# Kernel tuning notes

Measured on AMD Instinct MI355X. Metric: run time of the kernel, lower is better.

Reference implementation:

```python
import jax, jax.numpy as jnp
import numpy as np

UB = 35.0      # per-coordinate upper bound
SUM = 150.0    # equality constraint sum(z) = 150
NEG_SLOPE = 0.2


def _qp_project_one(v):
    """Solve min_z 0.5||z||^2 - v^T z  s.t. 0<=z<=UB, sum(z)=SUM  (n=5).
    Solution: z_i = clip(v_i - nu, 0, UB) with nu s.t. sum(z)=SUM.
    Exact closed form via the piecewise-linear breakpoints of g(nu)=sum(clip(v-nu,0,UB)).
    This matches QPFunction(Q=I, p=x, G,h box, A,b simplex) with v = -x."""
    bp = jnp.concatenate([v, v - UB])              # [10] breakpoints of g(nu)
    bs = jnp.sort(bp)[::-1]                        # descending in nu; g nondecreasing
    mid = 0.5 * (bs[:-1] + bs[1:])                 # [9] segment midpoints
    free = (v[None, :] > mid[:, None]) & (v[None, :] < mid[:, None] + UB)
    upper = v[None, :] >= mid[:, None] + UB
    nfree = jnp.sum(free, axis=1)
    num = jnp.sum(jnp.where(free, v[None, :], 0.0), axis=1) + UB * jnp.sum(upper, axis=1) - SUM
    nu_cand = num / jnp.maximum(nfree, 1)
    valid = (nfree > 0) & (nu_cand <= bs[:-1] + 1e-6) & (nu_cand >= bs[1:] - 1e-6)
    nu = nu_cand[jnp.argmax(valid)]
    return jnp.clip(v - nu, 0.0, UB)


def setup_inputs() -> dict:
    key = jax.random.key(0)
    ks = jax.random.split(key, 7)
    B, S, A = 65536, 17, 5
    state = jax.random.normal(ks[0], (B, S), dtype=jnp.float32)
    W1 = jax.random.normal(ks[1], (400, S), dtype=jnp.float32) * 0.05
    b1 = jax.random.normal(ks[2], (400,), dtype=jnp.float32) * 0.05
    W2 = jax.random.normal(ks[3], (300, 400), dtype=jnp.float32) * 0.05
    b2 = jax.random.normal(ks[4], (300,), dtype=jnp.float32) * 0.05
    W3 = jax.random.normal(ks[5], (A, 300), dtype=jnp.float32) * 0.05
    b3 = jax.random.normal(ks[6], (A,), dtype=jnp.float32) * 0.05
    return {"state": state, "W1": W1, "b1": b1, "W2": W2, "b2": b2,
            "W3": W3, "b3": b3, "training": 0}


def reference(state, W1, b1, W2, b2, W3, b3, training):
    lrelu = lambda x: jax.nn.leaky_relu(x, NEG_SLOPE)
    a = lrelu(state @ W1.T + b1)
    a = lrelu(a @ W2.T + b2)
    scaled_a = lrelu(a @ W3.T + b3)            # [B, 5]
    # QPFunction is called with linear term p = scaled_a, so v = -scaled_a
    opt_a = jax.vmap(_qp_project_one)(-scaled_a)
    return opt_a
```

## Files before the change

kernel.cpp:

```cpp
#include <hip/hip_runtime.h>
#include <hip/hip_bf16.h>

typedef __bf16 bf16x8 __attribute__((ext_vector_type(8)));
typedef float  f32x4  __attribute__((ext_vector_type(4)));
typedef long   long2v __attribute__((ext_vector_type(2)));

#define UBV   35.0f
#define SUMC  150.0f

__device__ __forceinline__ float lrelu(float x) { return fmaxf(x, 0.2f * x); }

__device__ __forceinline__ unsigned pkword(float a, float b, float c, float d) {
    unsigned w = (unsigned)__builtin_amdgcn_cvt_pk_fp8_f32(a, b, 0, false);
    w = (unsigned)__builtin_amdgcn_cvt_pk_fp8_f32(c, d, (int)w, true);
    return w;
}
__device__ __forceinline__ long mk64(unsigned lo, unsigned hi) {
    return (long)(((unsigned long long)hi << 32) | (unsigned long long)lo);
}
__device__ __forceinline__ void async16(void* lds_uniform, const void* gsrc) {
    __builtin_amdgcn_global_load_lds(
        (__attribute__((address_space(1))) void*)(gsrc),
        (__attribute__((address_space(3))) void*)(lds_uniform),
        16, 0, 0);
}


__global__ void prep_kernel(const float* __restrict__ W1, const float* __restrict__ b1,
                            const float* __restrict__ W2, const float* __restrict__ b2,
                            const float* __restrict__ W3, const float* __restrict__ b3,
                            __bf16* __restrict__ w1p, uint2* __restrict__ w2p,
                            uint2* __restrict__ w3c)
{
    int idx = blockIdx.x * blockDim.x + threadIdx.x;
    if (idx < 1664) {
        int lane = idx & 63;
        int nt = idx >> 6;
        int c16 = lane & 15, g = lane >> 4;
        int kk = nt >> 1, hh = nt & 1;
        int kap = kk * 32 + (c16 >> 2) * 8 + hh * 4 + (c16 & 3);
        bf16x8 v;
        #pragma unroll
        for (int j = 0; j < 8; ++j) {
            int k = g * 8 + j;
            float x = 0.f;
            if (kap < 400) {
                if (k < 17) x = W1[kap * 17 + k];
                else if (k == 17) x = b1[kap];
            } else if (kap == 400) {
                if (k == 17) x = 1.0f;
            }
            v[j] = (__bf16)x;
        }
        *(bf16x8*)(w1p + idx * 8) = v;
    } else if (idx < 1664 + 16640) {
        int i2 = idx - 1664;
        int fg = i2 >> 6, lane = i2 & 63;
        int q = fg / 65, rem = fg % 65;
        int t = rem / 13, kt = rem % 13;
        int c16 = lane & 15, g = lane >> 4;
        int local = t * 16 + c16;
        int ff = q * 79 + local;
        float v[8];
        #pragma unroll
        for (int j = 0; j < 8; ++j) {
            int kap = kt * 32 + g * 8 + j;
            float x = 0.f;
            if (local == 79) {
                x = (kap == 400) ? 1.0f : 0.f;
            } else if (local < 79 && ff < 300) {
                if (kap < 400) x = W2[ff * 400 + kap];
                else if (kap == 400) x = b2[ff];
            }
            v[j] = x;
        }
        uint2 d;
        d.x = pkword(v[0], v[1], v[2], v[3]);
        d.y = pkword(v[4], v[5], v[6], v[7]);
        int within = (kt < 12) ? ((kt >> 1) * 128 + lane * 2 + (kt & 1))
                               : (768 + lane);
        w2p[(q * 5 + t) * 832 + within] = d;
    } else if (idx < 1664 + 16640 + 768) {
        int i3 = idx - 1664 - 16640;
        int fg = i3 >> 6, lane = i3 & 63;
        int q = fg / 3, k2 = fg % 3;
        int o = lane & 15, g = lane >> 4;
        float v[8];
        #pragma unroll
        for (int j = 0; j < 8; ++j) {
            int t2  = 2 * k2 + (j >> 2);
            int rho = g * 4 + (j & 3);
            int local = t2 * 16 + rho;
            float x = 0.f;
            if (o < 5 && t2 < 5) {
                if (local == 79) x = b3[o] * 0.25f;
                else if (local < 79 && q * 79 + local < 300)
                    x = W3[o * 300 + q * 79 + local];
            }
            v[j] = x;
        }
        uint2 d;
        d.x = pkword(v[0], v[1], v[2], v[3]);
        d.y = pkword(v[4], v[5], v[6], v[7]);
        w3c[i3] = d;
    }
}

__global__ __launch_bounds__(256, 1)
void actor_kernel(const float* __restrict__ state,
                  const __bf16* __restrict__ w1p,
                  const uint2* __restrict__ w2p,
                  const uint2* __restrict__ w3c,
                  float* __restrict__ out)
{
    __shared__ __align__(16) char s_mem[2][33792];

    const int tid = threadIdx.x;
    const int wid = tid >> 6;
    const int ln  = tid & 63;
    const int g   = ln >> 4, c16 = ln & 15;
    const int brow = blockIdx.x << 7;

    {
        const char* gb1 = (const char*)w1p;
        #pragma unroll
        for (int i = wid; i < 26; i += 4)
            async16(&s_mem[0][0] + i * 1024, gb1 + i * 1024 + ln * 16);
        const char* gb2 = (const char*)w2p;
        #pragma unroll
        for (int i = wid; i < 33; i += 4)
            async16(&s_mem[1][0] + i * 1024, gb2 + i * 1024 + ln * 16);
    }

    bf16x8 sbA, sbB;
    {
        const float* spA = state + (brow + wid * 32 + c16) * 17;
        const float* spB = spA + 16 * 17;
        if (g == 0) {
            #pragma unroll
            for (int j = 0; j < 8; ++j) { sbA[j] = (__bf16)spA[j]; sbB[j] = (__bf16)spB[j]; }
        } else if (g == 1) {
            #pragma unroll
            for (int j = 0; j < 8; ++j) { sbA[j] = (__bf16)spA[8 + j]; sbB[j] = (__bf16)spB[8 + j]; }
        } else if (g == 2) {
            sbA[0] = (__bf16)spA[16]; sbB[0] = (__bf16)spB[16];
            sbA[1] = (__bf16)1.0f;    sbB[1] = (__bf16)1.0f;
            #pragma unroll
            for (int j = 2; j < 8; ++j) { sbA[j] = (__bf16)0.f; sbB[j] = (__bf16)0.f; }
        } else {
            #pragma unroll
            for (int j = 0; j < 8; ++j) { sbA[j] = (__bf16)0.f; sbB[j] = (__bf16)0.f; }
        }
    }

    long w3r[4][3];
    {
        const long* gw3 = (const long*)w3c;
        #pragma unroll
        for (int q = 0; q < 4; ++q)
            #pragma unroll
            for (int k2 = 0; k2 < 3; ++k2)
                w3r[q][k2] = gw3[(q * 3 + k2) * 64 + ln];
    }

    __syncthreads();

    long frvA[13], frvB[13];
    #pragma unroll
    for (int kt = 0; kt < 13; ++kt) {
        bf16x8 we = *(const bf16x8*)(&s_mem[0][0] + ((2 * kt) * 64 + ln) * 16);
        bf16x8 wo = *(const bf16x8*)(&s_mem[0][0] + ((2 * kt + 1) * 64 + ln) * 16);
        f32x4 aeA = {0.f,0.f,0.f,0.f}, aoA = {0.f,0.f,0.f,0.f};
        f32x4 aeB = {0.f,0.f,0.f,0.f}, aoB = {0.f,0.f,0.f,0.f};
        aeA = __builtin_amdgcn_mfma_f32_16x16x32_bf16(we, sbA, aeA, 0, 0, 0);
        aoA = __builtin_amdgcn_mfma_f32_16x16x32_bf16(wo, sbA, aoA, 0, 0, 0);
        aeB = __builtin_amdgcn_mfma_f32_16x16x32_bf16(we, sbB, aeB, 0, 0, 0);
        aoB = __builtin_amdgcn_mfma_f32_16x16x32_bf16(wo, sbB, aoB, 0, 0, 0);
        frvA[kt] = mk64(
            pkword(lrelu(aeA[0]), lrelu(aeA[1]), lrelu(aeA[2]), lrelu(aeA[3])),
            pkword(lrelu(aoA[0]), lrelu(aoA[1]), lrelu(aoA[2]), lrelu(aoA[3])));
        frvB[kt] = mk64(
            pkword(lrelu(aeB[0]), lrelu(aeB[1]), lrelu(aeB[2]), lrelu(aeB[3])),
            pkword(lrelu(aoB[0]), lrelu(aoB[1]), lrelu(aoB[2]), lrelu(aoB[3])));
    }

    __syncthreads();

    f32x4 ccsA = {0.f, 0.f, 0.f, 0.f};
    f32x4 ccsB = {0.f, 0.f, 0.f, 0.f};

    #pragma unroll 1
    for (int q = 0; q < 4; ++q) {
        if (q < 3) {
            char* lb = &s_mem[q & 1][0];
            const char* gb = (const char*)w2p + (q + 1) * 33280;
            #pragma unroll
            for (int i = wid; i < 33; i += 4)
                async16(lb + i * 1024, gb + i * 1024 + ln * 16);
        }

        const char* bufp = &s_mem[(q & 1) ^ 1][0];
        unsigned wdA[5], wdB[5];
        #pragma unroll
        for (int t = 0; t < 5; ++t) {
            const char* bt = bufp + t * 6656;
            f32x4 aA = {0.f,0.f,0.f,0.f}, aB = {0.f,0.f,0.f,0.f};
            #pragma unroll
            for (int kt2 = 0; kt2 < 6; ++kt2) {
                long2v p = *(const long2v*)(bt + kt2 * 1024 + ln * 16);
                aA = __builtin_amdgcn_mfma_f32_16x16x32_fp8_fp8(p[0], frvA[2 * kt2],     aA, 0, 0, 0);
                aB = __builtin_amdgcn_mfma_f32_16x16x32_fp8_fp8(p[0], frvB[2 * kt2],     aB, 0, 0, 0);
                aA = __builtin_amdgcn_mfma_f32_16x16x32_fp8_fp8(p[1], frvA[2 * kt2 + 1], aA, 0, 0, 0);
                aB = __builtin_amdgcn_mfma_f32_16x16x32_fp8_fp8(p[1], frvB[2 * kt2 + 1], aB, 0, 0, 0);
            }
            long p12 = *(const long*)(bt + 6144 + ln * 8);
            aA = __builtin_amdgcn_mfma_f32_16x16x32_fp8_fp8(p12, frvA[12], aA, 0, 0, 0);
            aB = __builtin_amdgcn_mfma_f32_16x16x32_fp8_fp8(p12, frvB[12], aB, 0, 0, 0);
            wdA[t] = pkword(lrelu(aA[0]), lrelu(aA[1]), lrelu(aA[2]), lrelu(aA[3]));
            wdB[t] = pkword(lrelu(aB[0]), lrelu(aB[1]), lrelu(aB[2]), lrelu(aB[3]));
        }
        {
            f32x4 cc = {0.f, 0.f, 0.f, 0.f};
            cc = __builtin_amdgcn_mfma_f32_16x16x32_fp8_fp8(w3r[q][0], mk64(wdA[0], wdA[1]), cc, 0, 0, 0);
            cc = __builtin_amdgcn_mfma_f32_16x16x32_fp8_fp8(w3r[q][1], mk64(wdA[2], wdA[3]), cc, 0, 0, 0);
            cc = __builtin_amdgcn_mfma_f32_16x16x32_fp8_fp8(w3r[q][2], mk64(wdA[4], 0u),     cc, 0, 0, 0);
            ccsA += cc;
        }
        {
            f32x4 cc = {0.f, 0.f, 0.f, 0.f};
            cc = __builtin_amdgcn_mfma_f32_16x16x32_fp8_fp8(w3r[q][0], mk64(wdB[0], wdB[1]), cc, 0, 0, 0);
            cc = __builtin_amdgcn_mfma_f32_16x16x32_fp8_fp8(w3r[q][1], mk64(wdB[2], wdB[3]), cc, 0, 0, 0);
            cc = __builtin_amdgcn_mfma_f32_16x16x32_fp8_fp8(w3r[q][2], mk64(wdB[4], 0u),     cc, 0, 0, 0);
            ccsB += cc;
        }
        if (q < 3) __syncthreads();
    }

    float tA4 = __shfl_xor(ccsA[0], 16);
    float sB0 = __shfl_xor(ccsB[0], 16);
    float sB1 = __shfl_xor(ccsB[1], 16);
    float sB2 = __shfl_xor(ccsB[2], 16);
    float sB3 = __shfl_xor(ccsB[3], 16);

    if (ln < 32) {
        float v[5];
        if (ln < 16) {
            v[0] = -lrelu(ccsA[0]); v[1] = -lrelu(ccsA[1]);
            v[2] = -lrelu(ccsA[2]); v[3] = -lrelu(ccsA[3]);
            v[4] = -lrelu(tA4);
        } else {
            v[0] = -lrelu(sB0); v[1] = -lrelu(sB1);
            v[2] = -lrelu(sB2); v[3] = -lrelu(sB3);
            v[4] = -lrelu(ccsB[0]);
        }

        float bp[10];
        #pragma unroll
        for (int i = 0; i < 5; ++i) { bp[i] = v[i]; bp[i + 5] = v[i] - UBV; }
        float blo = -1e30f, glo = 0.f;
        #pragma unroll
        for (int j = 0; j < 10; ++j) {
            float b = bp[j];
            float gsum = 0.f;
            #pragma unroll
            for (int i = 0; i < 5; ++i) {
                float zc = v[i] - b;
                zc = fminf(fmaxf(zc, 0.f), UBV);
                gsum += zc;
            }
            if (gsum >= SUMC && b > blo) { blo = b; glo = gsum; }
        }
        float bhi = 1e30f;
        #pragma unroll
        for (int j = 0; j < 10; ++j) {
            float b = bp[j];
            if (b > blo && b < bhi) bhi = b;
        }
        float mid = 0.5f * (blo + bhi);
        int nfree = 0;
        #pragma unroll
        for (int i = 0; i < 5; ++i)
            nfree += (v[i] > mid && v[i] < mid + UBV) ? 1 : 0;
        float nu = (nfree > 0) ? blo + (glo - SUMC) / (float)nfree : blo;

        int row = brow + wid * 32 + ln;
        #pragma unroll
        for (int o = 0; o < 5; ++o) {
            float zf = v[o] - nu;
            zf = fminf(fmaxf(zf, 0.f), UBV);
            out[row * 5 + o] = zf;
        }
    }
}

extern "C" void kernel_launch(void* const* d_in, const int* in_sizes, int n_in,
                              void* d_out, int out_size, void* d_ws, size_t ws_size,
                              hipStream_t stream) {
    const float* state = (const float*)d_in[0];
    const float* W1    = (const float*)d_in[1];
    const float* b1    = (const float*)d_in[2];
    const float* W2    = (const float*)d_in[3];
    const float* b2    = (const float*)d_in[4];
    const float* W3    = (const float*)d_in[5];
    const float* b3    = (const float*)d_in[6];
    float* out = (float*)d_out;

    char* base = (char*)d_ws;
    __bf16* w1p = (__bf16*)base;
    uint2*  w2p = (uint2*)(base + 26624);
    uint2*  w3c = (uint2*)(base + 26624 + 133120);

    const int total = 1664 + 16640 + 768;
    prep_kernel<<<(total + 255) / 256, 256, 0, stream>>>(W1, b1, W2, b2, W3, b3,
                                                         w1p, w2p, w3c);

    int B = in_sizes[0] / 17;
    actor_kernel<<<B / 128, 256, 0, stream>>>(state, w1p, w2p, w3c, out);
}
```

Baseline: 28.59 us.

## Split layer-2 output quarters across two wave groups with LDS reduction

After: 30.41 us. 1.06x slower.

```diff
diff --git a/kernel.cpp b/kernel.cpp
--- a/kernel.cpp
+++ b/kernel.cpp
@@ -106,35 +106,33 @@
     }
 }
 
-__global__ __launch_bounds__(256, 1)
+__global__ __launch_bounds__(512, 4)
 void actor_kernel(const float* __restrict__ state,
                   const __bf16* __restrict__ w1p,
                   const uint2* __restrict__ w2p,
                   const uint2* __restrict__ w3c,
                   float* __restrict__ out)
 {
-    __shared__ __align__(16) char s_mem[2][33792];
+    __shared__ __align__(16) char s_buf[2][33792];
+    __shared__ float s_red[2][4][32][8];
 
     const int tid = threadIdx.x;
     const int wid = tid >> 6;
     const int ln  = tid & 63;
     const int g   = ln >> 4, c16 = ln & 15;
-    const int brow = blockIdx.x << 7;
-
-    {
-        const char* gb1 = (const char*)w1p;
-        #pragma unroll
-        for (int i = wid; i < 26; i += 4)
-            async16(&s_mem[0][0] + i * 1024, gb1 + i * 1024 + ln * 16);
-        const char* gb2 = (const char*)w2p;
-        #pragma unroll
-        for (int i = wid; i < 33; i += 4)
-            async16(&s_mem[1][0] + i * 1024, gb2 + i * 1024 + ln * 16);
+    const int rg  = wid & 3;
+    const int qh  = wid >> 2;
+    const int brow = (blockIdx.x << 7) + rg * 32;
+
+    for (int b = 0; b < 2; ++b) {
+        const char* gb = (const char*)w2p + (b * 2) * 33280;
+        for (int i = wid; i < 33; i += 8)
+            async16(&s_buf[b][0] + i * 1024, gb + i * 1024 + ln * 16);
     }
 
     bf16x8 sbA, sbB;
     {
-        const float* spA = state + (brow + wid * 32 + c16) * 17;
+        const float* spA = state + (brow + c16) * 17;
         const float* spB = spA + 16 * 17;
         if (g == 0) {
             #pragma unroll
@@ -153,23 +151,21 @@
         }
     }
 
-    long w3r[4][3];
+    long w3r[2][3];
     {
         const long* gw3 = (const long*)w3c;
         #pragma unroll
-        for (int q = 0; q < 4; ++q)
+        for (int qi = 0; qi < 2; ++qi)
             #pragma unroll
             for (int k2 = 0; k2 < 3; ++k2)
-                w3r[q][k2] = gw3[(q * 3 + k2) * 64 + ln];
-    }
-
-    __syncthreads();
+                w3r[qi][k2] = gw3[((qh * 2 + qi) * 3 + k2) * 64 + ln];
+    }
 
     long frvA[13], frvB[13];
     #pragma unroll
     for (int kt = 0; kt < 13; ++kt) {
-        bf16x8 we = *(const bf16x8*)(&s_mem[0][0] + ((2 * kt) * 64 + ln) * 16);
-        bf16x8 wo = *(const bf16x8*)(&s_mem[0][0] + ((2 * kt + 1) * 64 + ln) * 16);
+        bf16x8 we = *(const bf16x8*)(w1p + ((2 * kt) * 64 + ln) * 8);
+        bf16x8 wo = *(const bf16x8*)(w1p + ((2 * kt + 1) * 64 + ln) * 8);
         f32x4 aeA = {0.f,0.f,0.f,0.f}, aoA = {0.f,0.f,0.f,0.f};
         f32x4 aeB = {0.f,0.f,0.f,0.f}, aoB = {0.f,0.f,0.f,0.f};
         aeA = __builtin_amdgcn_mfma_f32_16x16x32_bf16(we, sbA, aeA, 0, 0, 0);
@@ -186,21 +182,9 @@
 
     __syncthreads();
 
-    f32x4 ccsA = {0.f, 0.f, 0.f, 0.f};
-    f32x4 ccsB = {0.f, 0.f, 0.f, 0.f};
-
-    #pragma unroll 1
-    for (int q = 0; q < 4; ++q) {
-        if (q < 3) {
-            char* lb = &s_mem[q & 1][0];
-            const char* gb = (const char*)w2p + (q + 1) * 33280;
-            #pragma unroll
-            for (int i = wid; i < 33; i += 4)
-                async16(lb + i * 1024, gb + i * 1024 + ln * 16);
-        }
-
-        const char* bufp = &s_mem[(q & 1) ^ 1][0];
-        unsigned wdA[5], wdB[5];
+    unsigned wdA[5], wdB[5];
+    auto consume_q = [&]() {
+        const char* bufp = &s_buf[qh][0];
         #pragma unroll
         for (int t = 0; t < 5; ++t) {
             const char* bt = bufp + t * 6656;
@@ -219,39 +203,56 @@
             wdA[t] = pkword(lrelu(aA[0]), lrelu(aA[1]), lrelu(aA[2]), lrelu(aA[3]));
             wdB[t] = pkword(lrelu(aB[0]), lrelu(aB[1]), lrelu(aB[2]), lrelu(aB[3]));
         }
-        {
-            f32x4 cc = {0.f, 0.f, 0.f, 0.f};
-            cc = __builtin_amdgcn_mfma_f32_16x16x32_fp8_fp8(w3r[q][0], mk64(wdA[0], wdA[1]), cc, 0, 0, 0);
-            cc = __builtin_amdgcn_mfma_f32_16x16x32_fp8_fp8(w3r[q][1], mk64(wdA[2], wdA[3]), cc, 0, 0, 0);
-            cc = __builtin_amdgcn_mfma_f32_16x16x32_fp8_fp8(w3r[q][2], mk64(wdA[4], 0u),     cc, 0, 0, 0);
-            ccsA += cc;
-        }
-        {
-            f32x4 cc = {0.f, 0.f, 0.f, 0.f};
-            cc = __builtin_amdgcn_mfma_f32_16x16x32_fp8_fp8(w3r[q][0], mk64(wdB[0], wdB[1]), cc, 0, 0, 0);
-            cc = __builtin_amdgcn_mfma_f32_16x16x32_fp8_fp8(w3r[q][1], mk64(wdB[2], wdB[3]), cc, 0, 0, 0);
-            cc = __builtin_amdgcn_mfma_f32_16x16x32_fp8_fp8(w3r[q][2], mk64(wdB[4], 0u),     cc, 0, 0, 0);
-            ccsB += cc;
-        }
-        if (q < 3) __syncthreads();
-    }
-
-    float tA4 = __shfl_xor(ccsA[0], 16);
-    float sB0 = __shfl_xor(ccsB[0], 16);
-    float sB1 = __shfl_xor(ccsB[1], 16);
-    float sB2 = __shfl_xor(ccsB[2], 16);
-    float sB3 = __shfl_xor(ccsB[3], 16);
-
-    if (ln < 32) {
+    };
+    auto fold_q = [&](int qi, f32x4& cA, f32x4& cB) {
+        f32x4 cc = {0.f, 0.f, 0.f, 0.f};
+        cc = __builtin_amdgcn_mfma_f32_16x16x32_fp8_fp8(w3r[qi][0], mk64(wdA[0], wdA[1]), cc, 0, 0, 0);
+        cc = __builtin_amdgcn_mfma_f32_16x16x32_fp8_fp8(w3r[qi][1], mk64(wdA[2], wdA[3]), cc, 0, 0, 0);
+        cc = __builtin_amdgcn_mfma_f32_16x16x32_fp8_fp8(w3r[qi][2], mk64(wdA[4], 0u),     cc, 0, 0, 0);
+        cA += cc;
+        f32x4 cd = {0.f, 0.f, 0.f, 0.f};
+        cd = __builtin_amdgcn_mfma_f32_16x16x32_fp8_fp8(w3r[qi][0], mk64(wdB[0], wdB[1]), cd, 0, 0, 0);
+        cd = __builtin_amdgcn_mfma_f32_16x16x32_fp8_fp8(w3r[qi][1], mk64(wdB[2], wdB[3]), cd, 0, 0, 0);
+        cd = __builtin_amdgcn_mfma_f32_16x16x32_fp8_fp8(w3r[qi][2], mk64(wdB[4], 0u),     cd, 0, 0, 0);
+        cB += cd;
+    };
+
+    f32x4 ccsA = {0.f, 0.f, 0.f, 0.f};
+    f32x4 ccsB = {0.f, 0.f, 0.f, 0.f};
+
+    consume_q();
+    __syncthreads();
+
+    for (int b = 0; b < 2; ++b) {
+        const char* gb = (const char*)w2p + (b * 2 + 1) * 33280;
+        for (int i = wid; i < 33; i += 8)
+            async16(&s_buf[b][0] + i * 1024, gb + i * 1024 + ln * 16);
+    }
+    fold_q(0, ccsA, ccsB);
+
+    __syncthreads();
+
+    consume_q();
+    fold_q(1, ccsA, ccsB);
+
+    if (g == 0) {
+        #pragma unroll
+        for (int o = 0; o < 4; ++o) {
+            s_red[qh][rg][c16][o]      = ccsA[o];
+            s_red[qh][rg][16 + c16][o] = ccsB[o];
+        }
+    } else if (g == 1) {
+        s_red[qh][rg][c16][4]      = ccsA[0];
+        s_red[qh][rg][16 + c16][4] = ccsB[0];
+    }
+    __syncthreads();
+
+    if (qh == 0 && ln < 32) {
         float v[5];
-        if (ln < 16) {
-            v[0] = -lrelu(ccsA[0]); v[1] = -lrelu(ccsA[1]);
-            v[2] = -lrelu(ccsA[2]); v[3] = -lrelu(ccsA[3]);
-            v[4] = -lrelu(tA4);
-        } else {
-            v[0] = -lrelu(sB0); v[1] = -lrelu(sB1);
-            v[2] = -lrelu(sB2); v[3] = -lrelu(sB3);
-            v[4] = -lrelu(ccsB[0]);
+        #pragma unroll
+        for (int o = 0; o < 5; ++o) {
+            float s = s_red[0][rg][ln][o] + s_red[1][rg][ln][o];
+            v[o] = -lrelu(s);
         }
 
         float bp[10];
@@ -283,7 +284,7 @@
             nfree += (v[i] > mid && v[i] < mid + UBV) ? 1 : 0;
         float nu = (nfree > 0) ? blo + (glo - SUMC) / (float)nfree : blo;
 
-        int row = brow + wid * 32 + ln;
+        int row = brow + ln;
         #pragma unroll
         for (int o = 0; o < 5; ++o) {
             float zf = v[o] - nu;
@@ -315,5 +316,5 @@
                                                          w1p, w2p, w3c);
 
     int B = in_sizes[0] / 17;
-    actor_kernel<<<B / 128, 256, 0, stream>>>(state, w1p, w2p, w3c, out);
-}
+    actor_kernel<<<B / 128, 512, 0, stream>>>(state, w1p, w2p, w3c, out);
+}
```

## Use 16x16x128 scaled FP8 MFMA for layer-2 with re-laid-out weights

Applied to the files above, without the earlier changes.

Measured after the change: 26.67 us. -6.7%, faster.

```diff
diff --git a/kernel.cpp b/kernel.cpp
--- a/kernel.cpp
+++ b/kernel.cpp
@@ -4,9 +4,11 @@
 typedef __bf16 bf16x8 __attribute__((ext_vector_type(8)));
 typedef float  f32x4  __attribute__((ext_vector_type(4)));
 typedef long   long2v __attribute__((ext_vector_type(2)));
+typedef int    int8v  __attribute__((ext_vector_type(8)));
 
 #define UBV   35.0f
 #define SUMC  150.0f
+#define SCL1  0x7f7f7f7f
 
 __device__ __forceinline__ float lrelu(float x) { return fmaxf(x, 0.2f * x); }
 
@@ -36,9 +38,10 @@
     if (idx < 1664) {
         int lane = idx & 63;
         int nt = idx >> 6;
-        int c16 = lane & 15, g = lane >> 4;
-        int kk = nt >> 1, hh = nt & 1;
-        int kap = kk * 32 + (c16 >> 2) * 8 + hh * 4 + (c16 & 3);
+        int rho = lane & 15, g = lane >> 4;
+        int kap = (nt < 24)
+            ? 128 * (nt >> 3) + 32 * (rho >> 2) + 4 * (nt & 7) + (rho & 3)
+            : 384 + 8 * (rho >> 2) + 4 * (nt & 1) + (rho & 3);
         bf16x8 v;
         #pragma unroll
         for (int j = 0; j < 8; ++j) {
@@ -61,10 +64,19 @@
         int c16 = lane & 15, g = lane >> 4;
         int local = t * 16 + c16;
         int ff = q * 79 + local;
+        int within, kbase;
+        if (kt < 12) {
+            int m = kt >> 2, u = kt & 3;
+            kbase = 128 * m + 32 * g + 8 * u;
+            within = m * 256 + lane * 4 + u;
+        } else {
+            kbase = 384 + g * 8;
+            within = 768 + lane;
+        }
         float v[8];
         #pragma unroll
         for (int j = 0; j < 8; ++j) {
-            int kap = kt * 32 + g * 8 + j;
+            int kap = kbase + j;
             float x = 0.f;
             if (local == 79) {
                 x = (kap == 400) ? 1.0f : 0.f;
@@ -77,8 +89,6 @@
         uint2 d;
         d.x = pkword(v[0], v[1], v[2], v[3]);
         d.y = pkword(v[4], v[5], v[6], v[7]);
-        int within = (kt < 12) ? ((kt >> 1) * 128 + lane * 2 + (kt & 1))
-                               : (768 + lane);
         w2p[(q * 5 + t) * 832 + within] = d;
     } else if (idx < 1664 + 16640 + 768) {
         int i3 = idx - 1664 - 16640;
@@ -113,7 +123,7 @@
                   const uint2* __restrict__ w3c,
                   float* __restrict__ out)
 {
-    __shared__ __align__(16) char s_mem[2][33792];
+    __shared__ __align__(32) char s_mem[2][33792];
 
     const int tid = threadIdx.x;
     const int wid = tid >> 6;
@@ -165,23 +175,35 @@
 
     __syncthreads();
 
-    long frvA[13], frvB[13];
-    #pragma unroll
-    for (int kt = 0; kt < 13; ++kt) {
-        bf16x8 we = *(const bf16x8*)(&s_mem[0][0] + ((2 * kt) * 64 + ln) * 16);
-        bf16x8 wo = *(const bf16x8*)(&s_mem[0][0] + ((2 * kt + 1) * 64 + ln) * 16);
-        f32x4 aeA = {0.f,0.f,0.f,0.f}, aoA = {0.f,0.f,0.f,0.f};
-        f32x4 aeB = {0.f,0.f,0.f,0.f}, aoB = {0.f,0.f,0.f,0.f};
-        aeA = __builtin_amdgcn_mfma_f32_16x16x32_bf16(we, sbA, aeA, 0, 0, 0);
-        aoA = __builtin_amdgcn_mfma_f32_16x16x32_bf16(wo, sbA, aoA, 0, 0, 0);
-        aeB = __builtin_amdgcn_mfma_f32_16x16x32_bf16(we, sbB, aeB, 0, 0, 0);
-        aoB = __builtin_amdgcn_mfma_f32_16x16x32_bf16(wo, sbB, aoB, 0, 0, 0);
-        frvA[kt] = mk64(
-            pkword(lrelu(aeA[0]), lrelu(aeA[1]), lrelu(aeA[2]), lrelu(aeA[3])),
-            pkword(lrelu(aoA[0]), lrelu(aoA[1]), lrelu(aoA[2]), lrelu(aoA[3])));
-        frvB[kt] = mk64(
-            pkword(lrelu(aeB[0]), lrelu(aeB[1]), lrelu(aeB[2]), lrelu(aeB[3])),
-            pkword(lrelu(aoB[0]), lrelu(aoB[1]), lrelu(aoB[2]), lrelu(aoB[3])));
+    int8v fmA[3], fmB[3];
+    long fr12A, fr12B;
+    {
+        const __bf16* w1l = (const __bf16*)&s_mem[0][0];
+        #pragma unroll
+        for (int m = 0; m < 3; ++m)
+            #pragma unroll
+            for (int j = 0; j < 8; ++j) {
+                int nt = m * 8 + j;
+                bf16x8 w = *(const bf16x8*)(w1l + (nt * 64 + ln) * 8);
+                f32x4 aA = {0.f,0.f,0.f,0.f}, aB = {0.f,0.f,0.f,0.f};
+                aA = __builtin_amdgcn_mfma_f32_16x16x32_bf16(w, sbA, aA, 0, 0, 0);
+                aB = __builtin_amdgcn_mfma_f32_16x16x32_bf16(w, sbB, aB, 0, 0, 0);
+                fmA[m][j] = (int)pkword(lrelu(aA[0]), lrelu(aA[1]), lrelu(aA[2]), lrelu(aA[3]));
+                fmB[m][j] = (int)pkword(lrelu(aB[0]), lrelu(aB[1]), lrelu(aB[2]), lrelu(aB[3]));
+            }
+        unsigned dA[2], dB[2];
+        #pragma unroll
+        for (int h = 0; h < 2; ++h) {
+            int nt = 24 + h;
+            bf16x8 w = *(const bf16x8*)(w1l + (nt * 64 + ln) * 8);
+            f32x4 aA = {0.f,0.f,0.f,0.f}, aB = {0.f,0.f,0.f,0.f};
+            aA = __builtin_amdgcn_mfma_f32_16x16x32_bf16(w, sbA, aA, 0, 0, 0);
+            aB = __builtin_amdgcn_mfma_f32_16x16x32_bf16(w, sbB, aB, 0, 0, 0);
+            dA[h] = pkword(lrelu(aA[0]), lrelu(aA[1]), lrelu(aA[2]), lrelu(aA[3]));
+            dB[h] = pkword(lrelu(aB[0]), lrelu(aB[1]), lrelu(aB[2]), lrelu(aB[3]));
+        }
+        fr12A = mk64(dA[0], dA[1]);
+        fr12B = mk64(dB[0], dB[1]);
     }
 
     __syncthreads();
@@ -206,16 +228,16 @@
             const char* bt = bufp + t * 6656;
             f32x4 aA = {0.f,0.f,0.f,0.f}, aB = {0.f,0.f,0.f,0.f};
             #pragma unroll
-            for (int kt2 = 0; kt2 < 6; ++kt2) {
-                long2v p = *(const long2v*)(bt + kt2 * 1024 + ln * 16);
-                aA = __builtin_amdgcn_mfma_f32_16x16x32_fp8_fp8(p[0], frvA[2 * kt2],     aA, 0, 0, 0);
-                aB = __builtin_amdgcn_mfma_f32_16x16x32_fp8_fp8(p[0], frvB[2 * kt2],     aB, 0, 0, 0);
-                aA = __builtin_amdgcn_mfma_f32_16x16x32_fp8_fp8(p[1], frvA[2 * kt2 + 1], aA, 0, 0, 0);
-                aB = __builtin_amdgcn_mfma_f32_16x16x32_fp8_fp8(p[1], frvB[2 * kt2 + 1], aB, 0, 0, 0);
+            for (int m = 0; m < 3; ++m) {
+                int8v wf = *(const int8v*)(bt + m * 2048 + ln * 32);
+                aA = __builtin_amdgcn_mfma_scale_f32_16x16x128_f8f6f4(
+                         wf, fmA[m], aA, 0, 0, 0, SCL1, 0, SCL1);
+                aB = __builtin_amdgcn_mfma_scale_f32_16x16x128_f8f6f4(
+                         wf, fmB[m], aB, 0, 0, 0, SCL1, 0, SCL1);
             }
             long p12 = *(const long*)(bt + 6144 + ln * 8);
-            aA = __builtin_amdgcn_mfma_f32_16x16x32_fp8_fp8(p12, frvA[12], aA, 0, 0, 0);
-            aB = __builtin_amdgcn_mfma_f32_16x16x32_fp8_fp8(p12, frvB[12], aB, 0, 0, 0);
+            aA = __builtin_amdgcn_mfma_f32_16x16x32_fp8_fp8(p12, fr12A, aA, 0, 0, 0);
+            aB = __builtin_amdgcn_mfma_f32_16x16x32_fp8_fp8(p12, fr12B, aB, 0, 0, 0);
             wdA[t] = pkword(lrelu(aA[0]), lrelu(aA[1]), lrelu(aA[2]), lrelu(aA[3]));
             wdB[t] = pkword(lrelu(aB[0]), lrelu(aB[1]), lrelu(aB[2]), lrelu(aB[3]));
         }
```
